# Optimization experiments

Hardware: AMD Instinct MI355X
Metric: run time of the kernel (lower is better)

## Reference

```python
import jax, jax.numpy as jnp
from jax import lax
import numpy as np

V, D_EMB, H, P, B, T = 32000, 512, 1024, 512, 32, 512
NUM_LAYERS = 2


def setup_inputs() -> dict:
    key = jax.random.key(0)
    ks = jax.random.split(key, 2 + NUM_LAYERS * 5)
    tokens = jax.random.randint(ks[0], (B, T), 0, V, dtype=jnp.int32)
    embed = jax.random.normal(ks[1], (V, D_EMB), dtype=jnp.float32) * 0.02
    inp = {"tokens": tokens, "embed": embed}
    in_dims = [D_EMB] + [P] * (NUM_LAYERS - 1)
    for l in range(NUM_LAYERS):
        kk = ks[2 + 5 * l: 7 + 5 * l]
        inp[f"Wx{l}"] = jax.random.normal(kk[0], (in_dims[l], 4 * H), dtype=jnp.float32) * 0.02
        inp[f"Wh{l}"] = jax.random.normal(kk[1], (H, 4 * H), dtype=jnp.float32) * 0.02
        inp[f"b{l}"] = jnp.zeros((4 * H,), dtype=jnp.float32)
        inp[f"Wfc{l}"] = jax.random.normal(kk[3], (H, P), dtype=jnp.float32) * 0.02
        inp[f"bfc{l}"] = jnp.zeros((P,), dtype=jnp.float32)
    return inp


def _lstm(x, Wx, Wh, b):
    # x: [B, T, D] -> [B, T, H]. Keras gate order: i, f, g(cell), o.
    Bsz = x.shape[0]
    h0 = jnp.zeros((Bsz, H), dtype=x.dtype)
    c0 = jnp.zeros((Bsz, H), dtype=x.dtype)

    # Precompute input projection for all timesteps (one big GEMM).
    xz = jnp.einsum('btd,dg->btg', x, Wx) + b  # [B, T, 4H]

    def step(carry, zt):
        h, c = carry
        z = zt + h @ Wh
        i, f, g, o = jnp.split(z, 4, axis=-1)
        c = jax.nn.sigmoid(f) * c + jax.nn.sigmoid(i) * jnp.tanh(g)
        h = jax.nn.sigmoid(o) * jnp.tanh(c)
        return (h, c), h

    _, ys = lax.scan(step, (h0, c0), jnp.swapaxes(xz, 0, 1))  # ys: [T, B, H]
    return jnp.swapaxes(ys, 0, 1)


def reference(tokens, embed, Wx0, Wh0, b0, Wfc0, bfc0, Wx1, Wh1, b1, Wfc1, bfc1):
    # inference path: dropout is identity (training=False), use_softmax=False
    x = embed[tokens]  # [B, T, D_EMB]
    layers = [(Wx0, Wh0, b0, Wfc0, bfc0), (Wx1, Wh1, b1, Wfc1, bfc1)]
    for Wx, Wh, b, Wfc, bfc in layers:
        x = _lstm(x, Wx, Wh, b)
        x = x @ Wfc + bfc  # per-layer dense projection [B, T, P]
    return x
```

## Files before the change

kernel.cpp:

```cpp
#include <hip/hip_runtime.h>
#include <cstdio>
#include <cstdint>

typedef unsigned short u16;
typedef unsigned int u32;
typedef float f32x4 __attribute__((ext_vector_type(4)));
typedef short s16x8 __attribute__((ext_vector_type(8)));

#define DI __device__ __forceinline__

#define BATCH 32
#define SEQT 512
#define HDIM 1024
#define PDIM 512
#define DEMB 512
#define G4H 4096

DI u16 f2bf(float f) {
  u32 u = __float_as_uint(f);
  return (u16)((u + 0x7fffu + ((u >> 16) & 1u)) >> 16);
}
DI float bf2f(u16 h) { return __uint_as_float(((u32)h) << 16); }
DI void split2(float f, u16 &hi, u16 &lo) {
  hi = f2bf(f);
  lo = f2bf(f - bf2f(hi));
}
DI f32x4 mfma16(s16x8 a, s16x8 b, f32x4 c) {
  return __builtin_amdgcn_mfma_f32_16x16x32_bf16(a, b, c, 0, 0, 0);
}
DI void dma16(const void *g, void *l) {
  __builtin_amdgcn_global_load_lds((const __attribute__((address_space(1))) void *)g,
                                   (__attribute__((address_space(3))) void *)l, 16, 0, 0);
}
DI s16x8 ld128_dev(const u16 *p) {
  s16x8 r;
  asm volatile("global_load_dwordx4 %0, %1, off sc1" : "=v"(r) : "v"(p));
  return r;
}
DI void st16_dev(u16 *p, u16 v) {
  asm volatile("global_store_short %0, %1, off sc1" ::"v"(p), "v"((u32)v) : "memory");
}
DI void st32_dev(int *p, int v) {
  asm volatile("global_store_dword %0, %1, off sc1" ::"v"(p), "v"(v) : "memory");
}

#if __has_builtin(__builtin_amdgcn_exp2f) && __has_builtin(__builtin_amdgcn_rcpf)
DI float fsig(float x) {
  return __builtin_amdgcn_rcpf(1.f + __builtin_amdgcn_exp2f(-1.4426950408889634f * x));
}
DI float ftanh(float x) {
  return 2.f * __builtin_amdgcn_rcpf(1.f + __builtin_amdgcn_exp2f(-2.8853900817779268f * x)) - 1.f;
}
#else
DI float fsig(float x) { return 1.f / (1.f + expf(-x)); }
DI float ftanh(float x) { return tanhf(x); }
#endif

__global__ void k_gather_pack(const int *__restrict__ tokens, const float *__restrict__ embed,
                              u16 *__restrict__ xhi, u16 *__restrict__ xlo) {
  int idx = blockIdx.x * 256 + threadIdx.x;
  int m = idx >> 6;
  int k8 = (idx & 63) << 3;
  int tok = tokens[m];
  const float *src = embed + (size_t)tok * DEMB + k8;
  float4 a = *(const float4 *)src;
  float4 b = *(const float4 *)(src + 4);
  float v[8] = {a.x, a.y, a.z, a.w, b.x, b.y, b.z, b.w};
  union UV { u16 h[8]; int4 v; };
  UV uh, ul;
#pragma unroll
  for (int j = 0; j < 8; ++j) split2(v[j], uh.h[j], ul.h[j]);
  size_t o = (size_t)m * DEMB + k8;
  *(int4 *)(xhi + o) = uh.v;
  *(int4 *)(xlo + o) = ul.v;
}

__global__ void k_packT(const float *__restrict__ W, u16 *__restrict__ Thi, u16 *__restrict__ Tlo,
                        int K, int N) {
  __shared__ float tile[32][33];
  int n0 = blockIdx.x * 32, k0 = blockIdx.y * 32;
  int tx = threadIdx.x, ty = threadIdx.y;
#pragma unroll
  for (int i = 0; i < 4; ++i) tile[ty + 8 * i][tx] = W[(size_t)(k0 + ty + 8 * i) * N + n0 + tx];
  __syncthreads();
#pragma unroll
  for (int i = 0; i < 4; ++i) {
    int n = ty + 8 * i;
    u16 hi, lo;
    split2(tile[tx][n], hi, lo);
    size_t o = (size_t)(n0 + n) * K + k0 + tx;
    Thi[o] = hi;
    Tlo[o] = lo;
  }
}

__global__ void k_split(const float *__restrict__ W, u16 *__restrict__ hi, u16 *__restrict__ lo,
                        int n) {
  int i = blockIdx.x * 256 + threadIdx.x;
  if (i < n) split2(W[i], hi[i], lo[i]);
}

__global__ void k_beff(const float *__restrict__ bfc0, const float *__restrict__ Wx1,
                       const float *__restrict__ b1, float *__restrict__ beff) {
  int n = blockIdx.x * 256 + threadIdx.x;
  float acc = b1[n];
  for (int j = 0; j < PDIM; ++j) acc += bfc0[j] * Wx1[(size_t)j * G4H + n];
  beff[n] = acc;
}

template <int OM, int SA>
__global__ __launch_bounds__(256, 2) void k_gemm(const u16 *__restrict__ Ahi, const u16 *__restrict__ Alo,
                                                 const u16 *__restrict__ Bhi, const u16 *__restrict__ Blo,
                                                 const float *__restrict__ bias, void *__restrict__ out0,
                                                 int M, int N, int K) {
  __shared__ u16 sP[4][128 * 64];
  const int tid = threadIdx.x;
  const int w = tid >> 6, lane = tid & 63;
  const int la15 = lane & 15, la4 = lane >> 4;
  const int nbn = N >> 7;
  const int bm = blockIdx.x / nbn, bn = blockIdx.x % nbn;
  const u16 *src = (w == 0) ? Ahi : (w == 1) ? Alo : (w == 2) ? Bhi : Blo;
  const int rowbase = (w < 2) ? bm * 128 : bn * 128;
  char *lds = (char *)&sP[w][0];

  if (SA) {
    for (int i = tid; i < 2048; i += 256) ((unsigned long long *)&sP[1][0])[i] = 0ULL;
  }

  f32x4 acc[2][8] = {};
  for (int kb = 0; kb < K; kb += 64) {
    if (!(SA && w == 1)) {
#pragma unroll
      for (int i = 0; i < 16; ++i) {
        int s = i * 64 + lane;
        int row = s >> 3;
        int k16 = (s & 7) ^ (row & 7);
        dma16(src + (size_t)(rowbase + row) * K + kb + k16 * 8, lds + i * 1024);
      }
    }
    asm volatile("s_waitcnt vmcnt(0)" ::: "memory");
    __syncthreads();
#pragma unroll
    for (int ksl = 0; ksl < 2; ++ksl) {
      s16x8 ah[2], al[2];
#pragma unroll
      for (int rf = 0; rf < 2; ++rf) {
        int row = 32 * w + 16 * rf + la15;
        int slot = row * 8 + ((4 * ksl + la4) ^ (row & 7));
        ah[rf] = *(const s16x8 *)((const char *)&sP[0][0] + slot * 16);
        al[rf] = *(const s16x8 *)((const char *)&sP[1][0] + slot * 16);
      }
#pragma unroll
      for (int cf = 0; cf < 8; ++cf) {
        int col = 16 * cf + la15;
        int slot = col * 8 + ((4 * ksl + la4) ^ (col & 7));
        s16x8 bh = *(const s16x8 *)((const char *)&sP[2][0] + slot * 16);
        s16x8 bl = *(const s16x8 *)((const char *)&sP[3][0] + slot * 16);
#pragma unroll
        for (int rf = 0; rf < 2; ++rf) {
          acc[rf][cf] = mfma16(ah[rf], bh, acc[rf][cf]);
          acc[rf][cf] = mfma16(ah[rf], bl, acc[rf][cf]);
          acc[rf][cf] = mfma16(al[rf], bh, acc[rf][cf]);
        }
      }
    }
    __syncthreads();
  }
#pragma unroll
  for (int rf = 0; rf < 2; ++rf) {
#pragma unroll
    for (int cf = 0; cf < 8; ++cf) {
      int c = bn * 128 + 16 * cf + la15;
      float bv = bias ? bias[c] : 0.f;
#pragma unroll
      for (int q = 0; q < 4; ++q) {
        int r = bm * 128 + 32 * w + 16 * rf + 4 * la4 + q;
        float v = acc[rf][cf][q] + bv;
        if (OM == 0) {
          ((u16 *)out0)[(size_t)r * N + c] = f2bf(v);
        } else {
          int b2 = r & 31, tt = r >> 5;
          ((float *)out0)[((size_t)b2 * SEQT + tt) * PDIM + c] = v;
        }
      }
    }
  }
}

__global__ __launch_bounds__(256, 1) void k_recur_pipe(
    const u16 *__restrict__ xz0, const float *__restrict__ Wh0, const float *__restrict__ Wh1,
    const u16 *__restrict__ Weff, const float *__restrict__ beff,
    u16 *h0h, u16 *h1h, int *flags) {
  __shared__ u16 sW[32 * 1024];
  __shared__ u16 sE[32 * 1024];
  __shared__ float zacc[4][32][33];
  __shared__ float sC[256];
  const int tid = threadIdx.x;
  const int w = tid >> 6, lane = tid & 63;
  const int la15 = lane & 15, la4 = lane >> 4;
  const int wg = blockIdx.x;
  const int layer = wg >> 7;
  const int g = wg & 127;

  const float *Wh = layer ? Wh1 : Wh0;
  for (int i2 = tid; i2 < 32 * 1024; i2 += 256) {
    int zc = i2 & 31;
    int k = i2 >> 5;
    int gcol = (zc >> 3) * HDIM + 8 * g + (zc & 7);
    int boff = zc * 2048 + ((((k >> 3) ^ (zc & 7))) << 4) + (k & 7) * 2;
    *(u16 *)((char *)sW + boff) = f2bf(Wh[(size_t)k * G4H + gcol]);
    if (layer) *(u16 *)((char *)sE + boff) = Weff[(size_t)k * G4H + gcol];
  }
  sC[tid] = 0.f;
  __syncthreads();

  const int r_g = tid >> 3, hc = tid & 7;
  const int ks0 = 8 * w;
  u16 *histW = layer ? h1h : h0h;

  float bef[4] = {0.f, 0.f, 0.f, 0.f};
  if (layer) {
#pragma unroll
    for (int gi = 0; gi < 4; ++gi) bef[gi] = beff[gi * HDIM + 8 * g + hc];
  }

  for (int t = 0; t < SEQT; ++t) {
    float xzv[4] = {0.f, 0.f, 0.f, 0.f};
    if (!layer) {
      const u16 *px = xz0 + ((size_t)r_g * SEQT + t) * G4H + 8 * g + hc;
#pragma unroll
      for (int gi = 0; gi < 4; ++gi) xzv[gi] = bf2f(px[(size_t)gi * HDIM]);
    }
    if (w == 0) {
      if (!layer) {
        if (t > 0) {
          const int *dp = flags + lane;
          for (long tries = 0;; ++tries) {
            int a = __hip_atomic_load(dp, __ATOMIC_RELAXED, __HIP_MEMORY_SCOPE_AGENT);
            int b = __hip_atomic_load(dp + 64, __ATOMIC_RELAXED, __HIP_MEMORY_SCOPE_AGENT);
            if (__all(a >= t && b >= t)) break;
            if (tries > (1L << 22)) break;
            __builtin_amdgcn_s_sleep(1);
          }
        }
      } else {
        const int *d0 = flags + lane;
        const int *d1 = flags + 128 + lane;
        for (long tries = 0;; ++tries) {
          int a = __hip_atomic_load(d0, __ATOMIC_RELAXED, __HIP_MEMORY_SCOPE_AGENT);
          int b = __hip_atomic_load(d0 + 64, __ATOMIC_RELAXED, __HIP_MEMORY_SCOPE_AGENT);
          bool ok = (a >= t + 1 && b >= t + 1);
          if (t > 0) {
            int c = __hip_atomic_load(d1, __ATOMIC_RELAXED, __HIP_MEMORY_SCOPE_AGENT);
            int d = __hip_atomic_load(d1 + 64, __ATOMIC_RELAXED, __HIP_MEMORY_SCOPE_AGENT);
            ok = ok && (c >= t && d >= t);
          }
          if (__all(ok)) break;
          if (tries > (1L << 22)) break;
          __builtin_amdgcn_s_sleep(1);
        }
      }
    }
    __syncthreads();

    const bool doWh = (t > 0);
    const size_t tm1 = doWh ? (size_t)(t - 1) : 0;
    const u16 *pAwh = (layer ? h1h : h0h) + tm1 * 32 * HDIM;
    const u16 *pAwe = h0h + (size_t)t * 32 * HDIM;

#pragma unroll
    for (int rt = 0; rt < 2; ++rt) {
      const int row = 16 * rt + la15;
      s16x8 aw[8], ae[8];
      if (doWh) {
#pragma unroll
        for (int j8 = 0; j8 < 8; ++j8)
          aw[j8] = ld128_dev(pAwh + (size_t)row * HDIM + 32 * (ks0 + j8) + 8 * la4);
      }
      if (layer) {
#pragma unroll
        for (int j8 = 0; j8 < 8; ++j8)
          ae[j8] = ld128_dev(pAwe + (size_t)row * HDIM + 32 * (ks0 + j8) + 8 * la4);
      }
      if (doWh || layer) {
        asm volatile("s_waitcnt vmcnt(0)" ::: "memory");
        __builtin_amdgcn_sched_barrier(0);
        f32x4 acc[2] = {};
#pragma unroll
        for (int j8 = 0; j8 < 8; ++j8) {
#pragma unroll
          for (int cf = 0; cf < 2; ++cf) {
            int zc = 16 * cf + la15;
            int slot = (4 * (ks0 + j8) + la4) ^ (zc & 7);
            int boff = zc * 2048 + (slot << 4);
            if (doWh) acc[cf] = mfma16(aw[j8], *(const s16x8 *)((const char *)sW + boff), acc[cf]);
            if (layer) acc[cf] = mfma16(ae[j8], *(const s16x8 *)((const char *)sE + boff), acc[cf]);
          }
        }
#pragma unroll
        for (int cf = 0; cf < 2; ++cf)
#pragma unroll
          for (int q = 0; q < 4; ++q)
            zacc[w][16 * rt + 4 * la4 + q][16 * cf + la15] = acc[cf][q];
      }
    }
    __syncthreads();
    {
      float z4[4];
#pragma unroll
      for (int gi = 0; gi < 4; ++gi) {
        float s = layer ? bef[gi] : xzv[gi];
        if (t > 0 || layer) {
          int zc = gi * 8 + hc;
          s += zacc[0][r_g][zc] + zacc[1][r_g][zc] + zacc[2][r_g][zc] + zacc[3][r_g][zc];
        }
        z4[gi] = s;
      }
      float ig = fsig(z4[0]);
      float fg = fsig(z4[1]);
      float gg = ftanh(z4[2]);
      float og = fsig(z4[3]);
      float c = fg * sC[tid] + ig * gg;
      sC[tid] = c;
      float h = og * ftanh(c);
      st16_dev(histW + ((size_t)t * 32 + r_g) * HDIM + 8 * g + hc, f2bf(h));
    }
    asm volatile("s_waitcnt vmcnt(0)" ::: "memory");
    __syncthreads();
    if (tid == 0) st32_dev(flags + 128 * layer + g, t + 1);
  }
}

extern "C" void kernel_launch(void *const *d_in, const int *in_sizes, int n_in,
                              void *d_out, int out_size, void *d_ws, size_t ws_size,
                              hipStream_t stream) {
  const int *tokens = (const int *)d_in[0];
  const float *embed = (const float *)d_in[1];
  const float *Wx0 = (const float *)d_in[2];
  const float *Wh0 = (const float *)d_in[3];
  const float *b0 = (const float *)d_in[4];
  const float *Wfc0 = (const float *)d_in[5];
  const float *bfc0 = (const float *)d_in[6];
  const float *Wx1 = (const float *)d_in[7];
  const float *Wh1 = (const float *)d_in[8];
  const float *b1 = (const float *)d_in[9];
  const float *Wfc1 = (const float *)d_in[10];
  const float *bfc1 = (const float *)d_in[11];

  constexpr size_t NEED = 255856640;
  if (ws_size < NEED) {
    fprintf(stderr, "RNNLM kernel: ws too small (%zu < %zu)\n", ws_size, NEED);
    return;
  }
  char *ws = (char *)d_ws;
  u16 *xz0 = (u16 *)(ws + 0);
  u16 *h0h = (u16 *)(ws + 134217728);
  u16 *h1h = (u16 *)(ws + 167772160);
  u16 *x0hi = (u16 *)(ws + 201326592);
  u16 *x0lo = (u16 *)(ws + 218103808);
  u16 *Weff = (u16 *)(ws + 201326592);
  u16 *Wfc0hi = (u16 *)(ws + 209715200);
  u16 *Wfc0lo = (u16 *)(ws + 210763776);
  u16 *WfcT1hi = (u16 *)(ws + 211812352);
  u16 *WfcT1lo = (u16 *)(ws + 212860928);
  float *beff = (float *)(ws + 213909504);
  int *flags = (int *)(ws + 213925888);
  u16 *WxT0hi = (u16 *)(ws + 234881024);
  u16 *WxT0lo = (u16 *)(ws + 239075328);
  u16 *WxT1hi = (u16 *)(ws + 243269632);
  u16 *WxT1lo = (u16 *)(ws + 247463936);

  k_packT<<<dim3(G4H / 32, DEMB / 32), dim3(32, 8), 0, stream>>>(Wx0, WxT0hi, WxT0lo, DEMB, G4H);
  k_packT<<<dim3(G4H / 32, DEMB / 32), dim3(32, 8), 0, stream>>>(Wx1, WxT1hi, WxT1lo, DEMB, G4H);
  k_gather_pack<<<4096, 256, 0, stream>>>(tokens, embed, x0hi, x0lo);
  k_gemm<0, 0><<<dim3(128 * 32), 256, 0, stream>>>(x0hi, x0lo, WxT0hi, WxT0lo, b0, xz0,
                                                   16384, G4H, DEMB);
  k_split<<<2048, 256, 0, stream>>>(Wfc0, Wfc0hi, Wfc0lo, HDIM * PDIM);
  k_packT<<<dim3(PDIM / 32, HDIM / 32), dim3(32, 8), 0, stream>>>(Wfc1, WfcT1hi, WfcT1lo, HDIM, PDIM);
  k_beff<<<16, 256, 0, stream>>>(bfc0, Wx1, b1, beff);
  (void)hipMemsetAsync(flags, 0, 256 * sizeof(int), stream);
  k_gemm<0, 0><<<dim3(8 * 32), 256, 0, stream>>>(Wfc0hi, Wfc0lo, WxT1hi, WxT1lo, nullptr, Weff,
                                                 1024, G4H, PDIM);
  {
    const u16 *a0 = xz0; const float *a1 = Wh0; const float *a2 = Wh1;
    const u16 *a3 = Weff; const float *a4 = beff;
    u16 *a5 = h0h; u16 *a6 = h1h; int *a7 = flags;
    void *args[] = {&a0, &a1, &a2, &a3, &a4, &a5, &a6, &a7};
    hipError_t e = hipLaunchCooperativeKernel((void *)k_recur_pipe, dim3(256), dim3(256), args, 0, stream);
    if (e != hipSuccess) fprintf(stderr, "coop launch failed: %d\n", (int)e);
  }
  k_gemm<2, 1><<<dim3(128 * 4), 256, 0, stream>>>(h1h, h1h, WfcT1hi, WfcT1lo, bfc1, d_out,
                                                  16384, PDIM, HDIM);
}
```

Baseline: 5.652 ms.

## Move layer-1 input projection into layer-0 blocks via ring buffer of partial sums

Layer-0 blocks now compute the h0·Weff product for layer 1 alongside their own recurrence. They write fp32 per-wave partial sums into a 16-slot ring buffer in workspace, and layer-1 blocks only read and reduce those partials. Layer-0 waits on layer-1 progress so it never overwrites unread slots. This takes the second MFMA chain off layer 1's per-step critical path and balances work between the two layers. The cost is extra global fp32 stores and loads, more flag coupling between layers, and one extra layer-0 iteration at t=SEQT.

```diff
diff --git a/kernel.cpp b/kernel.cpp
--- a/kernel.cpp
+++ b/kernel.cpp
@@ -37,11 +37,19 @@
   asm volatile("global_load_dwordx4 %0, %1, off sc1" : "=v"(r) : "v"(p));
   return r;
 }
+DI f32x4 ldf4_dev(const float *p) {
+  f32x4 r;
+  asm volatile("global_load_dwordx4 %0, %1, off sc1" : "=v"(r) : "v"(p));
+  return r;
+}
 DI void st16_dev(u16 *p, u16 v) {
   asm volatile("global_store_short %0, %1, off sc1" ::"v"(p), "v"((u32)v) : "memory");
 }
 DI void st32_dev(int *p, int v) {
   asm volatile("global_store_dword %0, %1, off sc1" ::"v"(p), "v"(v) : "memory");
+}
+DI void st128f_dev(float *p, f32x4 v) {
+  asm volatile("global_store_dwordx4 %0, %1, off sc1" ::"v"(p), "v"(v) : "memory");
 }
 
 #if __has_builtin(__builtin_amdgcn_exp2f) && __has_builtin(__builtin_amdgcn_rcpf)
@@ -190,11 +198,12 @@
 __global__ __launch_bounds__(256, 1) void k_recur_pipe(
     const u16 *__restrict__ xz0, const float *__restrict__ Wh0, const float *__restrict__ Wh1,
     const u16 *__restrict__ Weff, const float *__restrict__ beff,
-    u16 *h0h, u16 *h1h, int *flags) {
+    u16 *h0h, u16 *h1h, float *zeffP, int *flags) {
   __shared__ u16 sW[32 * 1024];
   __shared__ u16 sE[32 * 1024];
   __shared__ float zacc[4][32][33];
   __shared__ float sC[256];
+  __shared__ float zE[32][33];
   const int tid = threadIdx.x;
   const int w = tid >> 6, lane = tid & 63;
   const int la15 = lane & 15, la4 = lane >> 4;
@@ -209,125 +218,233 @@
     int gcol = (zc >> 3) * HDIM + 8 * g + (zc & 7);
     int boff = zc * 2048 + ((((k >> 3) ^ (zc & 7))) << 4) + (k & 7) * 2;
     *(u16 *)((char *)sW + boff) = f2bf(Wh[(size_t)k * G4H + gcol]);
-    if (layer) *(u16 *)((char *)sE + boff) = Weff[(size_t)k * G4H + gcol];
+    if (!layer) *(u16 *)((char *)sE + boff) = Weff[(size_t)k * G4H + gcol];
   }
   sC[tid] = 0.f;
   __syncthreads();
 
   const int r_g = tid >> 3, hc = tid & 7;
   const int ks0 = 8 * w;
-  u16 *histW = layer ? h1h : h0h;
-
-  float bef[4] = {0.f, 0.f, 0.f, 0.f};
-  if (layer) {
-#pragma unroll
-    for (int gi = 0; gi < 4; ++gi) bef[gi] = beff[gi * HDIM + 8 * g + hc];
-  }
-
-  for (int t = 0; t < SEQT; ++t) {
-    float xzv[4] = {0.f, 0.f, 0.f, 0.f};
-    if (!layer) {
-      const u16 *px = xz0 + ((size_t)r_g * SEQT + t) * G4H + 8 * g + hc;
-#pragma unroll
-      for (int gi = 0; gi < 4; ++gi) xzv[gi] = bf2f(px[(size_t)gi * HDIM]);
-    }
-    if (w == 0) {
-      if (!layer) {
-        if (t > 0) {
-          const int *dp = flags + lane;
-          for (long tries = 0;; ++tries) {
-            int a = __hip_atomic_load(dp, __ATOMIC_RELAXED, __HIP_MEMORY_SCOPE_AGENT);
-            int b = __hip_atomic_load(dp + 64, __ATOMIC_RELAXED, __HIP_MEMORY_SCOPE_AGENT);
-            if (__all(a >= t && b >= t)) break;
-            if (tries > (1L << 22)) break;
-            __builtin_amdgcn_s_sleep(1);
-          }
-        }
-      } else {
-        const int *d0 = flags + lane;
-        const int *d1 = flags + 128 + lane;
+
+  if (!layer) {
+    for (int t = 0; t <= SEQT; ++t) {
+      const bool last = (t == SEQT);
+      float xzv[4] = {0.f, 0.f, 0.f, 0.f};
+      if (!last) {
+        const u16 *px = xz0 + ((size_t)r_g * SEQT + t) * G4H + 8 * g + hc;
+#pragma unroll
+        for (int gi = 0; gi < 4; ++gi) xzv[gi] = bf2f(px[(size_t)gi * HDIM]);
+      }
+      if (w == 0 && t > 0) {
+        const int *f0 = flags + lane;
+        const int *f1 = flags + 128 + lane;
+        const int bp = t - 16;
         for (long tries = 0;; ++tries) {
-          int a = __hip_atomic_load(d0, __ATOMIC_RELAXED, __HIP_MEMORY_SCOPE_AGENT);
-          int b = __hip_atomic_load(d0 + 64, __ATOMIC_RELAXED, __HIP_MEMORY_SCOPE_AGENT);
-          bool ok = (a >= t + 1 && b >= t + 1);
-          if (t > 0) {
-            int c = __hip_atomic_load(d1, __ATOMIC_RELAXED, __HIP_MEMORY_SCOPE_AGENT);
-            int d = __hip_atomic_load(d1 + 64, __ATOMIC_RELAXED, __HIP_MEMORY_SCOPE_AGENT);
-            ok = ok && (c >= t && d >= t);
+          int a = __hip_atomic_load(f0, __ATOMIC_RELAXED, __HIP_MEMORY_SCOPE_AGENT);
+          int b = __hip_atomic_load(f0 + 64, __ATOMIC_RELAXED, __HIP_MEMORY_SCOPE_AGENT);
+          bool ok = (a >= t && b >= t);
+          if (t > 16) {
+            int c = __hip_atomic_load(f1, __ATOMIC_RELAXED, __HIP_MEMORY_SCOPE_AGENT);
+            int d = __hip_atomic_load(f1 + 64, __ATOMIC_RELAXED, __HIP_MEMORY_SCOPE_AGENT);
+            ok = ok && (c >= bp && d >= bp);
           }
           if (__all(ok)) break;
           if (tries > (1L << 22)) break;
           __builtin_amdgcn_s_sleep(1);
         }
       }
-    }
-    __syncthreads();
-
-    const bool doWh = (t > 0);
-    const size_t tm1 = doWh ? (size_t)(t - 1) : 0;
-    const u16 *pAwh = (layer ? h1h : h0h) + tm1 * 32 * HDIM;
-    const u16 *pAwe = h0h + (size_t)t * 32 * HDIM;
-
-#pragma unroll
-    for (int rt = 0; rt < 2; ++rt) {
-      const int row = 16 * rt + la15;
-      s16x8 aw[8], ae[8];
-      if (doWh) {
+      __syncthreads();
+      if (t > 0) {
+        const u16 *pA = h0h + (size_t)(t - 1) * 32 * HDIM;
+        float *zb = zeffP + ((((size_t)((t - 1) & 15) * 128 + g) * 4 + w) << 10);
+        s16x8 aw0[8], aw1[8];
 #pragma unroll
         for (int j8 = 0; j8 < 8; ++j8)
-          aw[j8] = ld128_dev(pAwh + (size_t)row * HDIM + 32 * (ks0 + j8) + 8 * la4);
-      }
-      if (layer) {
+          aw0[j8] = ld128_dev(pA + (size_t)la15 * HDIM + 32 * (ks0 + j8) + 8 * la4);
 #pragma unroll
         for (int j8 = 0; j8 < 8; ++j8)
-          ae[j8] = ld128_dev(pAwe + (size_t)row * HDIM + 32 * (ks0 + j8) + 8 * la4);
-      }
-      if (doWh || layer) {
+          aw1[j8] = ld128_dev(pA + (size_t)(16 + la15) * HDIM + 32 * (ks0 + j8) + 8 * la4);
         asm volatile("s_waitcnt vmcnt(0)" ::: "memory");
         __builtin_amdgcn_sched_barrier(0);
-        f32x4 acc[2] = {};
-#pragma unroll
-        for (int j8 = 0; j8 < 8; ++j8) {
+        {
+          f32x4 acc0[2] = {}, accE[2] = {};
+#pragma unroll
+          for (int j8 = 0; j8 < 8; ++j8) {
+#pragma unroll
+            for (int cf = 0; cf < 2; ++cf) {
+              int zc = 16 * cf + la15;
+              int sl = (4 * (ks0 + j8) + la4) ^ (zc & 7);
+              int boff = zc * 2048 + (sl << 4);
+              if (!last) acc0[cf] = mfma16(aw0[j8], *(const s16x8 *)((const char *)sW + boff), acc0[cf]);
+              accE[cf] = mfma16(aw0[j8], *(const s16x8 *)((const char *)sE + boff), accE[cf]);
+            }
+          }
 #pragma unroll
           for (int cf = 0; cf < 2; ++cf) {
-            int zc = 16 * cf + la15;
-            int slot = (4 * (ks0 + j8) + la4) ^ (zc & 7);
-            int boff = zc * 2048 + (slot << 4);
-            if (doWh) acc[cf] = mfma16(aw[j8], *(const s16x8 *)((const char *)sW + boff), acc[cf]);
-            if (layer) acc[cf] = mfma16(ae[j8], *(const s16x8 *)((const char *)sE + boff), acc[cf]);
-          }
-        }
-#pragma unroll
-        for (int cf = 0; cf < 2; ++cf)
-#pragma unroll
-          for (int q = 0; q < 4; ++q)
-            zacc[w][16 * rt + 4 * la4 + q][16 * cf + la15] = acc[cf][q];
-      }
+            if (!last) {
+#pragma unroll
+              for (int q = 0; q < 4; ++q) zacc[w][4 * la4 + q][16 * cf + la15] = acc0[cf][q];
+            }
+            st128f_dev(zb + (16 * cf + la15) * 32 + 4 * la4, accE[cf]);
+          }
+        }
+        {
+          f32x4 acc0[2] = {}, accE[2] = {};
+#pragma unroll
+          for (int j8 = 0; j8 < 8; ++j8) {
+#pragma unroll
+            for (int cf = 0; cf < 2; ++cf) {
+              int zc = 16 * cf + la15;
+              int sl = (4 * (ks0 + j8) + la4) ^ (zc & 7);
+              int boff = zc * 2048 + (sl << 4);
+              if (!last) acc0[cf] = mfma16(aw1[j8], *(const s16x8 *)((const char *)sW + boff), acc0[cf]);
+              accE[cf] = mfma16(aw1[j8], *(const s16x8 *)((const char *)sE + boff), accE[cf]);
+            }
+          }
+#pragma unroll
+          for (int cf = 0; cf < 2; ++cf) {
+            if (!last) {
+#pragma unroll
+              for (int q = 0; q < 4; ++q) zacc[w][16 + 4 * la4 + q][16 * cf + la15] = acc0[cf][q];
+            }
+            st128f_dev(zb + (16 * cf + la15) * 32 + 16 + 4 * la4, accE[cf]);
+          }
+        }
+      }
+      __syncthreads();
+      if (!last) {
+        float z4[4];
+#pragma unroll
+        for (int gi = 0; gi < 4; ++gi) {
+          float s = xzv[gi];
+          if (t > 0) {
+            int zc = gi * 8 + hc;
+            s += zacc[0][r_g][zc] + zacc[1][r_g][zc] + zacc[2][r_g][zc] + zacc[3][r_g][zc];
+          }
+          z4[gi] = s;
+        }
+        float ig = fsig(z4[0]);
+        float fg = fsig(z4[1]);
+        float gg = ftanh(z4[2]);
+        float og = fsig(z4[3]);
+        float c = fg * sC[tid] + ig * gg;
+        sC[tid] = c;
+        float h = og * ftanh(c);
+        st16_dev(h0h + ((size_t)t * 32 + r_g) * HDIM + 8 * g + hc, f2bf(h));
+      }
+      asm volatile("s_waitcnt vmcnt(0)" ::: "memory");
+      __syncthreads();
+      if (tid == 0) st32_dev(flags + g, t + 1);
     }
-    __syncthreads();
-    {
-      float z4[4];
-#pragma unroll
-      for (int gi = 0; gi < 4; ++gi) {
-        float s = layer ? bef[gi] : xzv[gi];
-        if (t > 0 || layer) {
+  } else {
+    float bef[4];
+#pragma unroll
+    for (int gi = 0; gi < 4; ++gi) bef[gi] = beff[gi * HDIM + 8 * g + hc];
+    const int zc2 = tid >> 3, rowq = (tid & 7) << 2;
+    for (int t = 0; t < SEQT; ++t) {
+      if (w == 0) {
+        const int *f0 = flags + lane;
+        const int *f1 = flags + 128 + lane;
+        const int need0 = t + 2;
+        for (long tries = 0;; ++tries) {
+          int a = __hip_atomic_load(f0, __ATOMIC_RELAXED, __HIP_MEMORY_SCOPE_AGENT);
+          int b = __hip_atomic_load(f0 + 64, __ATOMIC_RELAXED, __HIP_MEMORY_SCOPE_AGENT);
+          bool ok = (a >= need0 && b >= need0);
+          if (t > 0) {
+            int c = __hip_atomic_load(f1, __ATOMIC_RELAXED, __HIP_MEMORY_SCOPE_AGENT);
+            int d = __hip_atomic_load(f1 + 64, __ATOMIC_RELAXED, __HIP_MEMORY_SCOPE_AGENT);
+            ok = ok && (c >= t && d >= t);
+          }
+          if (__all(ok)) break;
+          if (tries > (1L << 22)) break;
+          __builtin_amdgcn_s_sleep(1);
+        }
+      }
+      __syncthreads();
+      s16x8 aw0[8], aw1[8];
+      const u16 *pA = h1h + (size_t)(t - 1) * 32 * HDIM;
+      if (t > 0) {
+#pragma unroll
+        for (int j8 = 0; j8 < 8; ++j8)
+          aw0[j8] = ld128_dev(pA + (size_t)la15 * HDIM + 32 * (ks0 + j8) + 8 * la4);
+#pragma unroll
+        for (int j8 = 0; j8 < 8; ++j8)
+          aw1[j8] = ld128_dev(pA + (size_t)(16 + la15) * HDIM + 32 * (ks0 + j8) + 8 * la4);
+      }
+      const float *rb0 = zeffP + (((size_t)(t & 15) * 128 + g) << 12);
+      f32x4 zp0 = ldf4_dev(rb0 + zc2 * 32 + rowq);
+      f32x4 zp1 = ldf4_dev(rb0 + 1024 + zc2 * 32 + rowq);
+      f32x4 zp2 = ldf4_dev(rb0 + 2048 + zc2 * 32 + rowq);
+      f32x4 zp3 = ldf4_dev(rb0 + 3072 + zc2 * 32 + rowq);
+      asm volatile("s_waitcnt vmcnt(0)" ::: "memory");
+      __builtin_amdgcn_sched_barrier(0);
+      {
+        f32x4 s4 = zp0 + zp1 + zp2 + zp3;
+        zE[zc2][rowq + 0] = s4[0];
+        zE[zc2][rowq + 1] = s4[1];
+        zE[zc2][rowq + 2] = s4[2];
+        zE[zc2][rowq + 3] = s4[3];
+      }
+      if (t > 0) {
+        {
+          f32x4 acc0[2] = {};
+#pragma unroll
+          for (int j8 = 0; j8 < 8; ++j8) {
+#pragma unroll
+            for (int cf = 0; cf < 2; ++cf) {
+              int zc = 16 * cf + la15;
+              int sl = (4 * (ks0 + j8) + la4) ^ (zc & 7);
+              int boff = zc * 2048 + (sl << 4);
+              acc0[cf] = mfma16(aw0[j8], *(const s16x8 *)((const char *)sW + boff), acc0[cf]);
+            }
+          }
+#pragma unroll
+          for (int cf = 0; cf < 2; ++cf)
+#pragma unroll
+            for (int q = 0; q < 4; ++q) zacc[w][4 * la4 + q][16 * cf + la15] = acc0[cf][q];
+        }
+        {
+          f32x4 acc0[2] = {};
+#pragma unroll
+          for (int j8 = 0; j8 < 8; ++j8) {
+#pragma unroll
+            for (int cf = 0; cf < 2; ++cf) {
+              int zc = 16 * cf + la15;
+              int sl = (4 * (ks0 + j8) + la4) ^ (zc & 7);
+              int boff = zc * 2048 + (sl << 4);
+              acc0[cf] = mfma16(aw1[j8], *(const s16x8 *)((const char *)sW + boff), acc0[cf]);
+            }
+          }
+#pragma unroll
+          for (int cf = 0; cf < 2; ++cf)
+#pragma unroll
+            for (int q = 0; q < 4; ++q) zacc[w][16 + 4 * la4 + q][16 * cf + la15] = acc0[cf][q];
+        }
+      }
+      __syncthreads();
+      {
+        float z4[4];
+#pragma unroll
+        for (int gi = 0; gi < 4; ++gi) {
           int zc = gi * 8 + hc;
-          s += zacc[0][r_g][zc] + zacc[1][r_g][zc] + zacc[2][r_g][zc] + zacc[3][r_g][zc];
-        }
-        z4[gi] = s;
-      }
-      float ig = fsig(z4[0]);
-      float fg = fsig(z4[1]);
-      float gg = ftanh(z4[2]);
-      float og = fsig(z4[3]);
-      float c = fg * sC[tid] + ig * gg;
-      sC[tid] = c;
-      float h = og * ftanh(c);
-      st16_dev(histW + ((size_t)t * 32 + r_g) * HDIM + 8 * g + hc, f2bf(h));
+          float s = bef[gi] + zE[zc][r_g];
+          if (t > 0)
+            s += zacc[0][r_g][zc] + zacc[1][r_g][zc] + zacc[2][r_g][zc] + zacc[3][r_g][zc];
+          z4[gi] = s;
+        }
+        float ig = fsig(z4[0]);
+        float fg = fsig(z4[1]);
+        float gg = ftanh(z4[2]);
+        float og = fsig(z4[3]);
+        float c = fg * sC[tid] + ig * gg;
+        sC[tid] = c;
+        float h = og * ftanh(c);
+        st16_dev(h1h + ((size_t)t * 32 + r_g) * HDIM + 8 * g + hc, f2bf(h));
+      }
+      asm volatile("s_waitcnt vmcnt(0)" ::: "memory");
+      __syncthreads();
+      if (tid == 0) st32_dev(flags + 128 + g, t + 1);
     }
-    asm volatile("s_waitcnt vmcnt(0)" ::: "memory");
-    __syncthreads();
-    if (tid == 0) st32_dev(flags + 128 * layer + g, t + 1);
   }
 }
 
@@ -365,6 +482,7 @@
   u16 *WfcT1lo = (u16 *)(ws + 212860928);
   float *beff = (float *)(ws + 213909504);
   int *flags = (int *)(ws + 213925888);
+  float *zeffP = (float *)(ws + 218103808);
   u16 *WxT0hi = (u16 *)(ws + 234881024);
   u16 *WxT0lo = (u16 *)(ws + 239075328);
   u16 *WxT1hi = (u16 *)(ws + 243269632);
@@ -384,8 +502,8 @@
   {
     const u16 *a0 = xz0; const float *a1 = Wh0; const float *a2 = Wh1;
     const u16 *a3 = Weff; const float *a4 = beff;
-    u16 *a5 = h0h; u16 *a6 = h1h; int *a7 = flags;
-    void *args[] = {&a0, &a1, &a2, &a3, &a4, &a5, &a6, &a7};
+    u16 *a5 = h0h; u16 *a6 = h1h; float *a7 = zeffP; int *a8 = flags;
+    void *args[] = {&a0, &a1, &a2, &a3, &a4, &a5, &a6, &a7, &a8};
     hipError_t e = hipLaunchCooperativeKernel((void *)k_recur_pipe, dim3(256), dim3(256), args, 0, stream);
     if (e != hipSuccess) fprintf(stderr, "coop launch failed: %d\n", (int)e);
   }
```

Measured after the change: 5.199 ms. 8.0% less time.
